# Kernel tuning notes

Hardware: AMD Instinct MI355X
Metric: run time of the kernel (lower is better)

## Reference

```python
import jax, jax.numpy as jnp
import numpy as np

B, S, E, H, WIN = 8, 4096, 512, 8, 5
D = E // H
HALF = WIN // 2


def setup_inputs() -> dict:
    key = jax.random.key(0)
    ks = jax.random.split(key, 9)
    s = 1.0 / np.sqrt(E)
    return {
        "x": jax.random.normal(ks[0], (B, S, E), dtype=jnp.float32),
        "Wq": jax.random.normal(ks[1], (E, E), dtype=jnp.float32) * s,
        "Wk": jax.random.normal(ks[2], (E, E), dtype=jnp.float32) * s,
        "Wv": jax.random.normal(ks[3], (E, E), dtype=jnp.float32) * s,
        "bq": jax.random.normal(ks[4], (E,), dtype=jnp.float32) * 0.01,
        "bk": jax.random.normal(ks[5], (E,), dtype=jnp.float32) * 0.01,
        "bv": jax.random.normal(ks[6], (E,), dtype=jnp.float32) * 0.01,
        "Wo": jax.random.normal(ks[7], (E, E), dtype=jnp.float32) * s,
        "bo": jax.random.normal(ks[8], (E,), dtype=jnp.float32) * 0.01,
    }


def reference(x, Wq, Wk, Wv, bq, bk, bv, Wo, bo):
    # Sliding-window MHA: each position i attends to keys in [i-2, i+2] (clipped).
    b, s, e = x.shape
    h, d = H, e // H
    q = (x @ Wq.T + bq).reshape(b, s, h, d)
    k = (x @ Wk.T + bk).reshape(b, s, h, d)
    v = (x @ Wv.T + bv).reshape(b, s, h, d)
    pos = jnp.arange(s)[:, None] + jnp.arange(-HALF, HALF + 1)[None, :]
    valid = (pos >= 0) & (pos < s)
    idx = jnp.clip(pos, 0, s - 1)
    kw = k[:, idx]
    vw = v[:, idx]
    scale = 1.0 / jnp.sqrt(jnp.asarray(d, dtype=x.dtype))
    scores = jnp.einsum('bshd,bswhd->bhsw', q, kw) * scale
    scores = jnp.where(valid[None, None], scores, jnp.finfo(scores.dtype).min)
    attn = jax.nn.softmax(scores, axis=-1)
    out = jnp.einsum('bhsw,bswhd->bshd', attn, vw).reshape(b, s, e)
    return out @ Wo.T + bo
```

## Files before the change

kernel.cpp:

```cpp
#include <hip/hip_runtime.h>

#define S_ 4096

typedef __attribute__((ext_vector_type(8))) short short8;
typedef __attribute__((ext_vector_type(4))) float f32x4;

static __device__ __forceinline__ float bf2f(unsigned short u) {
  union { unsigned int i; float f; } v; v.i = ((unsigned int)u) << 16; return v.f;
}
static __device__ __forceinline__ unsigned short f2bf(float f) {
  union { float f; unsigned int i; } v; v.f = f;
  unsigned int r = v.i + 0x7FFFu + ((v.i >> 16) & 1u);
  return (unsigned short)(r >> 16);
}

#define LOAD_LDS16(g, l) __builtin_amdgcn_global_load_lds( \
    (const __attribute__((address_space(1))) void*)(g),     \
    (__attribute__((address_space(3))) void*)(l), 16, 0, 0)

__global__ __launch_bounds__(256) void cast_x_kernel(
    const float* __restrict__ x, unsigned short* __restrict__ xb) {
  int i = (blockIdx.x * 256 + threadIdx.x) * 4;
  float4 v = *(const float4*)(x + i);
  ushort4 o;
  o.x = f2bf(v.x); o.y = f2bf(v.y); o.z = f2bf(v.z); o.w = f2bf(v.w);
  *(ushort4*)(xb + i) = o;
}

__global__ __launch_bounds__(256) void cast_w_kernel(
    const float* __restrict__ Wq, const float* __restrict__ Wk,
    const float* __restrict__ Wv, const float* __restrict__ Wo,
    const float* __restrict__ bq, const float* __restrict__ bk,
    const float* __restrict__ bv,
    unsigned short* __restrict__ Wcat, unsigned short* __restrict__ Wob,
    float* __restrict__ bcat) {
  int i = blockIdx.x * 256 + threadIdx.x;
  Wcat[i]          = f2bf(Wq[i] * 0.125f);
  Wcat[262144 + i] = f2bf(Wk[i]);
  Wcat[524288 + i] = f2bf(Wv[i]);
  Wob[i]           = f2bf(Wo[i]);
  if (i < 512) { bcat[i] = bq[i] * 0.125f; bcat[512 + i] = bk[i]; bcat[1024 + i] = bv[i]; }
}

template<int OUT_BF16, int NBX>
__global__ __launch_bounds__(256, 2) void gemm128(
    const unsigned short* __restrict__ A,
    const unsigned short* __restrict__ Bw,
    const float* __restrict__ bias,
    void* __restrict__ Cv) {
  __shared__ unsigned short lds[32768];
  const int N = NBX * 128;
  const int NWG = 256 * NBX;

  const int tid = threadIdx.x;
  const int lane = tid & 63;
  const int wv = tid >> 6;
  const int wm = wv >> 1, wn = wv & 1;
  const int r = lane & 15, g = lane >> 4;

  int id = blockIdx.x;
  id = (id & 7) * (NWG >> 3) + (id >> 3);
  const int by = id / NBX, bx = id % NBX;
  const int m0 = by * 128, n0 = bx * 128;

  float bcol[4];
#pragma unroll
  for (int nj = 0; nj < 4; ++nj) bcol[nj] = bias[n0 + wn * 64 + nj * 16 + r];
  asm volatile("" : "+v"(bcol[0]), "+v"(bcol[1]), "+v"(bcol[2]), "+v"(bcol[3]));

  const unsigned short* gA[4];
  const unsigned short* gB[4];
  int ldsb[4];
#pragma unroll
  for (int i = 0; i < 4; ++i) {
    int ci = i * 256 + tid;
    int row = ci >> 3, sp = ci & 7;
    int cs = sp ^ (row & 7);
    gA[i] = A + (size_t)(m0 + row) * 512 + cs * 8;
    gB[i] = Bw + (size_t)(n0 + row) * 512 + cs * 8;
    ldsb[i] = (i * 256 + wv * 64) * 8;
  }

  f32x4 acc[4][4] = {};

#define STAGE(kt) do {                                         \
    unsigned short* tb_ = lds + (((kt) & 1) << 14);            \
    LOAD_LDS16(gA[0] + (kt) * 64, tb_ + ldsb[0]);              \
    LOAD_LDS16(gA[1] + (kt) * 64, tb_ + ldsb[1]);              \
    LOAD_LDS16(gA[2] + (kt) * 64, tb_ + ldsb[2]);              \
    LOAD_LDS16(gA[3] + (kt) * 64, tb_ + ldsb[3]);              \
    LOAD_LDS16(gB[0] + (kt) * 64, tb_ + 8192 + ldsb[0]);       \
    LOAD_LDS16(gB[1] + (kt) * 64, tb_ + 8192 + ldsb[1]);       \
    LOAD_LDS16(gB[2] + (kt) * 64, tb_ + 8192 + ldsb[2]);       \
    LOAD_LDS16(gB[3] + (kt) * 64, tb_ + 8192 + ldsb[3]);       \
  } while (0)

#define COMPUTE(kt) do {                                                     \
    const unsigned short* tb_ = lds + (((kt) & 1) << 14);                    \
    _Pragma("unroll") for (int ks = 0; ks < 2; ++ks) {                       \
      const int sw_ = ((ks * 4 + g) ^ (r & 7)) * 8;                          \
      short8 a_[4], b_[4];                                                   \
      _Pragma("unroll") for (int mi = 0; mi < 4; ++mi)                       \
        a_[mi] = *(const short8*)&tb_[(wm * 64 + mi * 16 + r) * 64 + sw_];   \
      _Pragma("unroll") for (int nj = 0; nj < 4; ++nj)                       \
        b_[nj] = *(const short8*)&tb_[8192 + (wn * 64 + nj * 16 + r) * 64 + sw_]; \
      _Pragma("unroll") for (int mi = 0; mi < 4; ++mi)                       \
        _Pragma("unroll") for (int nj = 0; nj < 4; ++nj)                     \
          acc[mi][nj] = __builtin_amdgcn_mfma_f32_16x16x32_bf16(             \
              a_[mi], b_[nj], acc[mi][nj], 0, 0, 0);                         \
    }                                                                        \
  } while (0)

  STAGE(0); STAGE(1);
  asm volatile("s_waitcnt vmcnt(8)" ::: "memory");
  __builtin_amdgcn_s_barrier();
  asm volatile("" ::: "memory");

  for (int t = 0; t < 6; ++t) {
    COMPUTE(t);
    asm volatile("s_waitcnt lgkmcnt(0)" ::: "memory");
    __builtin_amdgcn_s_barrier();
    asm volatile("" ::: "memory");
    STAGE(t + 2);
    asm volatile("s_waitcnt vmcnt(8)" ::: "memory");
    __builtin_amdgcn_s_barrier();
    asm volatile("" ::: "memory");
  }
  COMPUTE(6);
  asm volatile("s_waitcnt vmcnt(0)" ::: "memory");
  __builtin_amdgcn_s_barrier();
  asm volatile("" ::: "memory");
  COMPUTE(7);

#undef STAGE
#undef COMPUTE

  const int ldc = N;
#pragma unroll
  for (int nj = 0; nj < 4; ++nj) {
    const int col = n0 + wn * 64 + nj * 16 + r;
#pragma unroll
    for (int mi = 0; mi < 4; ++mi) {
      const int rowb = m0 + wm * 64 + mi * 16 + g * 4;
      f32x4 v = acc[mi][nj];
#pragma unroll
      for (int j = 0; j < 4; ++j) {
        float val = v[j] + bcol[nj];
        size_t off = (size_t)(rowb + j) * ldc + col;
        if (OUT_BF16) ((unsigned short*)Cv)[off] = f2bf(val);
        else          ((float*)Cv)[off] = val;
      }
    }
  }
}

__global__ __launch_bounds__(256) void swa_fused(
    const unsigned short* __restrict__ qkv, unsigned short* __restrict__ attn) {
  const int m = (blockIdx.x * 256 + threadIdx.x) >> 6;
  const int lane = threadIdx.x & 63;
  const int s = m & (S_ - 1);
  const unsigned short* base = qkv + (size_t)m * 1536 + lane * 8;

  float q[8];
  {
    short8 qv = *(const short8*)base;
#pragma unroll
    for (int j = 0; j < 8; ++j) q[j] = bf2f((unsigned short)qv[j]);
  }

  float sc[5];
#pragma unroll
  for (int w = 0; w < 5; ++w) {
    int s2 = s + w - 2;
    float p = -1e30f;
    if ((unsigned)s2 < (unsigned)S_) {
      short8 kv = *(const short8*)(base + (ptrdiff_t)(w - 2) * 1536 + 512);
      float a = 0.f;
#pragma unroll
      for (int j = 0; j < 8; ++j) a += q[j] * bf2f((unsigned short)kv[j]);
      a += __shfl_xor(a, 1);
      a += __shfl_xor(a, 2);
      a += __shfl_xor(a, 4);
      p = a;
    }
    sc[w] = p;
  }

  float mx = fmaxf(fmaxf(fmaxf(sc[0], sc[1]), fmaxf(sc[2], sc[3])), sc[4]);
  float e[5], sum = 0.f;
#pragma unroll
  for (int w = 0; w < 5; ++w) { e[w] = __expf(sc[w] - mx); sum += e[w]; }
  float inv = 1.0f / sum;

  float o[8] = {0.f, 0.f, 0.f, 0.f, 0.f, 0.f, 0.f, 0.f};
#pragma unroll
  for (int w = 0; w < 5; ++w) {
    int s2 = s + w - 2;
    if ((unsigned)s2 < (unsigned)S_) {
      short8 vv = *(const short8*)(base + (ptrdiff_t)(w - 2) * 1536 + 1024);
      float pw = e[w] * inv;
#pragma unroll
      for (int j = 0; j < 8; ++j) o[j] += pw * bf2f((unsigned short)vv[j]);
    }
  }

  short8 ov;
#pragma unroll
  for (int j = 0; j < 8; ++j) ov[j] = (short)f2bf(o[j]);
  *(short8*)(attn + (size_t)m * 512 + lane * 8) = ov;
}

extern "C" void kernel_launch(void* const* d_in, const int* in_sizes, int n_in,
                              void* d_out, int out_size, void* d_ws, size_t ws_size,
                              hipStream_t stream) {
  const float* x  = (const float*)d_in[0];
  const float* Wq = (const float*)d_in[1];
  const float* Wk = (const float*)d_in[2];
  const float* Wv = (const float*)d_in[3];
  const float* bq = (const float*)d_in[4];
  const float* bk = (const float*)d_in[5];
  const float* bv = (const float*)d_in[6];
  const float* Wo = (const float*)d_in[7];
  const float* bo = (const float*)d_in[8];
  float* out = (float*)d_out;

  char* ws = (char*)d_ws;
  unsigned short* xb   = (unsigned short*)(ws);
  unsigned short* qkv  = (unsigned short*)(ws + 33554432);
  unsigned short* attn = (unsigned short*)(ws + 134217728);
  unsigned short* Wcat = (unsigned short*)(ws + 167772160);
  unsigned short* Wob  = (unsigned short*)(ws + 169345024);
  float* bcat          = (float*)(ws + 169869312);

  cast_x_kernel<<<16384, 256, 0, stream>>>(x, xb);
  cast_w_kernel<<<1024, 256, 0, stream>>>(Wq, Wk, Wv, Wo, bq, bk, bv, Wcat, Wob, bcat);
  gemm128<1, 12><<<3072, 256, 0, stream>>>(xb, Wcat, bcat, qkv);
  swa_fused<<<8192, 256, 0, stream>>>(qkv, attn);
  gemm128<0, 4><<<1024, 256, 0, stream>>>(attn, Wob, bo, out);
}
```

Measured before the change: 243.1 us.

## Switch GEMMs to 256x256 tiles with 8 waves and fuse cast kernels

Both GEMMs now use 256x256 output tiles computed by 512-thread workgroups (8 waves, each covering 128x64), which doubles operand reuse per LDS byte. The K loop is restructured to issue the next stage's global-to-LDS loads early, interleave LDS fragment reads with MFMA groups, and raise wave priority around the MFMA bursts. The x and weight cast kernels are merged into one launch. The trade-offs are 128KB of LDS per workgroup, more accumulator registers, and fewer workgroups: 256 for the output projection, which may leave some CUs idle.

```diff
diff --git a/kernel.cpp b/kernel.cpp
--- a/kernel.cpp
+++ b/kernel.cpp
@@ -18,130 +18,145 @@
     (const __attribute__((address_space(1))) void*)(g),     \
     (__attribute__((address_space(3))) void*)(l), 16, 0, 0)
 
-__global__ __launch_bounds__(256) void cast_x_kernel(
-    const float* __restrict__ x, unsigned short* __restrict__ xb) {
-  int i = (blockIdx.x * 256 + threadIdx.x) * 4;
-  float4 v = *(const float4*)(x + i);
-  ushort4 o;
-  o.x = f2bf(v.x); o.y = f2bf(v.y); o.z = f2bf(v.z); o.w = f2bf(v.w);
-  *(ushort4*)(xb + i) = o;
-}
-
-__global__ __launch_bounds__(256) void cast_w_kernel(
+__global__ __launch_bounds__(256) void cast_all(
+    const float* __restrict__ x,
     const float* __restrict__ Wq, const float* __restrict__ Wk,
     const float* __restrict__ Wv, const float* __restrict__ Wo,
     const float* __restrict__ bq, const float* __restrict__ bk,
     const float* __restrict__ bv,
-    unsigned short* __restrict__ Wcat, unsigned short* __restrict__ Wob,
-    float* __restrict__ bcat) {
-  int i = blockIdx.x * 256 + threadIdx.x;
-  Wcat[i]          = f2bf(Wq[i] * 0.125f);
-  Wcat[262144 + i] = f2bf(Wk[i]);
-  Wcat[524288 + i] = f2bf(Wv[i]);
-  Wob[i]           = f2bf(Wo[i]);
-  if (i < 512) { bcat[i] = bq[i] * 0.125f; bcat[512 + i] = bk[i]; bcat[1024 + i] = bv[i]; }
+    unsigned short* __restrict__ xb, unsigned short* __restrict__ Wcat,
+    unsigned short* __restrict__ Wob, float* __restrict__ bcat) {
+  const int bid = blockIdx.x;
+  int i4 = (bid * 256 + threadIdx.x) * 4;
+  float4 v = *(const float4*)(x + i4);
+  ushort4 o;
+  o.x = f2bf(v.x); o.y = f2bf(v.y); o.z = f2bf(v.z); o.w = f2bf(v.w);
+  *(ushort4*)(xb + i4) = o;
+  if (bid < 1024) {
+    int i = bid * 256 + threadIdx.x;
+    Wcat[i]          = f2bf(Wq[i] * 0.125f);
+    Wcat[262144 + i] = f2bf(Wk[i]);
+    Wcat[524288 + i] = f2bf(Wv[i]);
+    Wob[i]           = f2bf(Wo[i]);
+    if (i < 512) { bcat[i] = bq[i] * 0.125f; bcat[512 + i] = bk[i]; bcat[1024 + i] = bv[i]; }
+  }
 }
 
 template<int OUT_BF16, int NBX>
-__global__ __launch_bounds__(256, 2) void gemm128(
+__global__ __launch_bounds__(512, 2) void gemm256(
     const unsigned short* __restrict__ A,
     const unsigned short* __restrict__ Bw,
     const float* __restrict__ bias,
     void* __restrict__ Cv) {
-  __shared__ unsigned short lds[32768];
-  const int N = NBX * 128;
-  const int NWG = 256 * NBX;
+  __shared__ unsigned short lds[65536];
+  const int N = NBX * 256;
+  const int NWG = 128 * NBX;
 
   const int tid = threadIdx.x;
   const int lane = tid & 63;
   const int wv = tid >> 6;
-  const int wm = wv >> 1, wn = wv & 1;
+  const int wm = wv >> 2;
+  const int wn = wv & 3;
   const int r = lane & 15, g = lane >> 4;
 
   int id = blockIdx.x;
   id = (id & 7) * (NWG >> 3) + (id >> 3);
   const int by = id / NBX, bx = id % NBX;
-  const int m0 = by * 128, n0 = bx * 128;
+  const int m0 = by * 256, n0 = bx * 256;
 
   float bcol[4];
 #pragma unroll
   for (int nj = 0; nj < 4; ++nj) bcol[nj] = bias[n0 + wn * 64 + nj * 16 + r];
   asm volatile("" : "+v"(bcol[0]), "+v"(bcol[1]), "+v"(bcol[2]), "+v"(bcol[3]));
 
-  const unsigned short* gA[4];
-  const unsigned short* gB[4];
-  int ldsb[4];
-#pragma unroll
-  for (int i = 0; i < 4; ++i) {
-    int ci = i * 256 + tid;
-    int row = ci >> 3, sp = ci & 7;
-    int cs = sp ^ (row & 7);
-    gA[i] = A + (size_t)(m0 + row) * 512 + cs * 8;
-    gB[i] = Bw + (size_t)(n0 + row) * 512 + cs * 8;
-    ldsb[i] = (i * 256 + wv * 64) * 8;
-  }
-
-  f32x4 acc[4][4] = {};
-
-#define STAGE(kt) do {                                         \
-    unsigned short* tb_ = lds + (((kt) & 1) << 14);            \
-    LOAD_LDS16(gA[0] + (kt) * 64, tb_ + ldsb[0]);              \
-    LOAD_LDS16(gA[1] + (kt) * 64, tb_ + ldsb[1]);              \
-    LOAD_LDS16(gA[2] + (kt) * 64, tb_ + ldsb[2]);              \
-    LOAD_LDS16(gA[3] + (kt) * 64, tb_ + ldsb[3]);              \
-    LOAD_LDS16(gB[0] + (kt) * 64, tb_ + 8192 + ldsb[0]);       \
-    LOAD_LDS16(gB[1] + (kt) * 64, tb_ + 8192 + ldsb[1]);       \
-    LOAD_LDS16(gB[2] + (kt) * 64, tb_ + 8192 + ldsb[2]);       \
-    LOAD_LDS16(gB[3] + (kt) * 64, tb_ + 8192 + ldsb[3]);       \
+  const int srow = lane >> 3;
+  const int scs = (lane & 7) ^ srow;
+  const unsigned short* gA = A + (size_t)(m0 + wv * 32 + srow) * 512 + scs * 8;
+  const unsigned short* gB = Bw + (size_t)(n0 + wv * 32 + srow) * 512 + scs * 8;
+  const int sdst = wv * 2048;
+
+  const int sw0 = ((0 + g) ^ (r & 7)) * 8;
+  const int sw1 = ((4 + g) ^ (r & 7)) * 8;
+  const int arow = (wm * 128 + r) * 64;
+  const int brow = 16384 + (wn * 64 + r) * 64;
+
+  f32x4 acc[8][4] = {};
+
+#define STAGE(kt) do {                                              \
+    unsigned short* tb_ = lds + (((kt) & 1) << 15);                 \
+    _Pragma("unroll") for (int i_ = 0; i_ < 4; ++i_) {              \
+      LOAD_LDS16(gA + (kt) * 64 + i_ * 4096, tb_ + sdst + i_ * 512);\
+      LOAD_LDS16(gB + (kt) * 64 + i_ * 4096, tb_ + 16384 + sdst + i_ * 512); \
+    }                                                               \
   } while (0)
 
-#define COMPUTE(kt) do {                                                     \
-    const unsigned short* tb_ = lds + (((kt) & 1) << 14);                    \
-    _Pragma("unroll") for (int ks = 0; ks < 2; ++ks) {                       \
-      const int sw_ = ((ks * 4 + g) ^ (r & 7)) * 8;                          \
-      short8 a_[4], b_[4];                                                   \
-      _Pragma("unroll") for (int mi = 0; mi < 4; ++mi)                       \
-        a_[mi] = *(const short8*)&tb_[(wm * 64 + mi * 16 + r) * 64 + sw_];   \
-      _Pragma("unroll") for (int nj = 0; nj < 4; ++nj)                       \
-        b_[nj] = *(const short8*)&tb_[8192 + (wn * 64 + nj * 16 + r) * 64 + sw_]; \
-      _Pragma("unroll") for (int mi = 0; mi < 4; ++mi)                       \
-        _Pragma("unroll") for (int nj = 0; nj < 4; ++nj)                     \
-          acc[mi][nj] = __builtin_amdgcn_mfma_f32_16x16x32_bf16(             \
-              a_[mi], b_[nj], acc[mi][nj], 0, 0, 0);                         \
-    }                                                                        \
-  } while (0)
-
-  STAGE(0); STAGE(1);
-  asm volatile("s_waitcnt vmcnt(8)" ::: "memory");
+  STAGE(0);
+  asm volatile("s_waitcnt vmcnt(0)" ::: "memory");
   __builtin_amdgcn_s_barrier();
-  asm volatile("" ::: "memory");
-
-  for (int t = 0; t < 6; ++t) {
-    COMPUTE(t);
+
+#pragma unroll 1
+  for (int t = 0; t < 8; ++t) {
+    const unsigned short* tb = lds + ((t & 1) << 15);
+
+    short8 a0[2][2], bfr[4][2];
+#pragma unroll
+    for (int d = 0; d < 2; ++d) {
+      a0[d][0] = *(const short8*)&tb[arow + d * 1024 + sw0];
+      a0[d][1] = *(const short8*)&tb[arow + d * 1024 + sw1];
+    }
+#pragma unroll
+    for (int nj = 0; nj < 4; ++nj) {
+      bfr[nj][0] = *(const short8*)&tb[brow + nj * 1024 + sw0];
+      bfr[nj][1] = *(const short8*)&tb[brow + nj * 1024 + sw1];
+    }
+    if (t < 7) STAGE(t + 1);
+    __builtin_amdgcn_s_barrier();
+    __builtin_amdgcn_s_setprio(1);
+#pragma unroll
+    for (int kk = 0; kk < 2; ++kk)
+#pragma unroll
+      for (int d = 0; d < 2; ++d)
+#pragma unroll
+        for (int nj = 0; nj < 4; ++nj)
+          acc[d][nj] = __builtin_amdgcn_mfma_f32_16x16x32_bf16(
+              a0[d][kk], bfr[nj][kk], acc[d][nj], 0, 0, 0);
+    __builtin_amdgcn_s_setprio(0);
     asm volatile("s_waitcnt lgkmcnt(0)" ::: "memory");
     __builtin_amdgcn_s_barrier();
-    asm volatile("" ::: "memory");
-    STAGE(t + 2);
-    asm volatile("s_waitcnt vmcnt(8)" ::: "memory");
-    __builtin_amdgcn_s_barrier();
-    asm volatile("" ::: "memory");
-  }
-  COMPUTE(6);
-  asm volatile("s_waitcnt vmcnt(0)" ::: "memory");
-  __builtin_amdgcn_s_barrier();
-  asm volatile("" ::: "memory");
-  COMPUTE(7);
-
+
+#pragma unroll
+    for (int q = 1; q < 4; ++q) {
+      short8 aq[2][2];
+#pragma unroll
+      for (int d = 0; d < 2; ++d) {
+        aq[d][0] = *(const short8*)&tb[arow + (2 * q + d) * 1024 + sw0];
+        aq[d][1] = *(const short8*)&tb[arow + (2 * q + d) * 1024 + sw1];
+      }
+      __builtin_amdgcn_s_barrier();
+      __builtin_amdgcn_s_setprio(1);
+#pragma unroll
+      for (int kk = 0; kk < 2; ++kk)
+#pragma unroll
+        for (int d = 0; d < 2; ++d)
+#pragma unroll
+          for (int nj = 0; nj < 4; ++nj)
+            acc[2 * q + d][nj] = __builtin_amdgcn_mfma_f32_16x16x32_bf16(
+                aq[d][kk], bfr[nj][kk], acc[2 * q + d][nj], 0, 0, 0);
+      __builtin_amdgcn_s_setprio(0);
+      if (q == 3) asm volatile("s_waitcnt vmcnt(0) lgkmcnt(0)" ::: "memory");
+      else        asm volatile("s_waitcnt lgkmcnt(0)" ::: "memory");
+      __builtin_amdgcn_s_barrier();
+    }
+  }
 #undef STAGE
-#undef COMPUTE
 
   const int ldc = N;
 #pragma unroll
   for (int nj = 0; nj < 4; ++nj) {
     const int col = n0 + wn * 64 + nj * 16 + r;
 #pragma unroll
-    for (int mi = 0; mi < 4; ++mi) {
-      const int rowb = m0 + wm * 64 + mi * 16 + g * 4;
+    for (int mi = 0; mi < 8; ++mi) {
+      const int rowb = m0 + wm * 128 + mi * 16 + g * 4;
       f32x4 v = acc[mi][nj];
 #pragma unroll
       for (int j = 0; j < 4; ++j) {
@@ -232,9 +247,9 @@
   unsigned short* Wob  = (unsigned short*)(ws + 169345024);
   float* bcat          = (float*)(ws + 169869312);
 
-  cast_x_kernel<<<16384, 256, 0, stream>>>(x, xb);
-  cast_w_kernel<<<1024, 256, 0, stream>>>(Wq, Wk, Wv, Wo, bq, bk, bv, Wcat, Wob, bcat);
-  gemm128<1, 12><<<3072, 256, 0, stream>>>(xb, Wcat, bcat, qkv);
+  cast_all<<<16384, 256, 0, stream>>>(x, Wq, Wk, Wv, Wo, bq, bk, bv,
+                                      xb, Wcat, Wob, bcat);
+  gemm256<1, 6><<<768, 512, 0, stream>>>(xb, Wcat, bcat, qkv);
   swa_fused<<<8192, 256, 0, stream>>>(qkv, attn);
-  gemm128<0, 4><<<1024, 256, 0, stream>>>(attn, Wob, bo, out);
-}
+  gemm256<0, 2><<<256, 512, 0, stream>>>(attn, Wob, bo, out);
+}
```

Result: slower. 285.3 us (+17.4%).
